# Optimization experiments

Measured on AMD Instinct MI355X. Metric: run time of the kernel, lower is better.

Reference implementation:

```python
import jax, jax.numpy as jnp
import numpy as np

IN_F = 8192
OUT_F = 8192
MAX_STATES = 100
THRESHOLD = MAX_STATES // 2  # 50


def setup_inputs() -> dict:
    key = jax.random.key(0)
    k1, k2 = jax.random.split(key, 2)
    spike_input = (jax.random.uniform(k1, (IN_F,)) < 0.2).astype(jnp.float32)
    # synapse states as in __init__: randn*5 + threshold, clamped to [1, max_states]
    synapse_states = jnp.clip(
        jax.random.normal(k2, (OUT_F, IN_F)) * 5.0 + THRESHOLD, 1.0, float(MAX_STATES)
    ).astype(jnp.float32)
    membrane_potential = jnp.zeros((OUT_F,), jnp.float32)
    adaptive_threshold = jnp.full((OUT_F,), 3.0, jnp.float32)
    eligibility_trace = jnp.zeros((OUT_F, IN_F), jnp.float32)
    refractory_period = jnp.zeros((OUT_F,), jnp.float32)
    return {
        "spike_input": spike_input,
        "synapse_states": synapse_states,
        "membrane_potential": membrane_potential,
        "adaptive_threshold": adaptive_threshold,
        "eligibility_trace": eligibility_trace,
        "refractory_period": refractory_period,
    }


def reference(spike_input, synapse_states, membrane_potential, adaptive_threshold,
              eligibility_trace, refractory_period):
    # Ternary (effectively binary 0/1) weights from synapse states
    w = (synapse_states > float(THRESHOLD)).astype(jnp.float32)  # [out, in]
    x = spike_input.reshape(-1)                                   # [in]
    current = w @ x                                               # [out]
    # LIF membrane update with refractory gating
    v_mem = membrane_potential * 0.5 + current * (1.0 - refractory_period * 0.5)
    spikes = (v_mem >= adaptive_threshold).astype(jnp.float32)    # [out]
    # Eligibility trace: decay + outer-product accumulation + clamp
    new_trace = jnp.clip(eligibility_trace * 0.8 + jnp.outer(spikes, x), 0.0, 5.0)
    # Refractory update
    new_refractory = jnp.clip(refractory_period + spikes - 0.1, 0.0, 1.0)
    # Membrane reset where spiked
    new_membrane = v_mem * (1.0 - spikes)
    return spikes, new_membrane, new_trace, new_refractory
```

## Files before the change

kernel.cpp:

```cpp
#include <hip/hip_runtime.h>


#define IN_F 8192
#define OUT_F 8192
#define BLOCK 256
#define ROW4 (IN_F / 4)
#define CHUNKS (ROW4 / 64)
#define PF 16

typedef float f32x4 __attribute__((ext_vector_type(4)));

__device__ __forceinline__ float dot_step(const f32x4 s, const f32x4 xv) {
    float a = 0.0f;
    a += (s[0] > 50.0f) ? xv[0] : 0.0f;
    a += (s[1] > 50.0f) ? xv[1] : 0.0f;
    a += (s[2] > 50.0f) ? xv[2] : 0.0f;
    a += (s[3] > 50.0f) ? xv[3] : 0.0f;
    return a;
}

__device__ __forceinline__ f32x4 trace_step(const f32x4 t, const f32x4 xv,
                                            const float spike) {
    f32x4 o;
    o[0] = fminf(fmaxf(t[0] * 0.8f + spike * xv[0], 0.0f), 5.0f);
    o[1] = fminf(fmaxf(t[1] * 0.8f + spike * xv[1], 0.0f), 5.0f);
    o[2] = fminf(fmaxf(t[2] * 0.8f + spike * xv[2], 0.0f), 5.0f);
    o[3] = fminf(fmaxf(t[3] * 0.8f + spike * xv[3], 0.0f), 5.0f);
    return o;
}

__global__ __launch_bounds__(BLOCK) void snn_fused_kernel(
    const f32x4* __restrict__ x4,
    const float* __restrict__ syn,
    const float* __restrict__ mem,
    const float* __restrict__ thr,
    const float* __restrict__ refr,
    const f32x4* __restrict__ tr4,
    float* __restrict__ out_spikes,
    float* __restrict__ out_mem,
    float* __restrict__ out_refr,
    f32x4* __restrict__ otr4)
{
    const int wave = threadIdx.x >> 6;
    const int lane = threadIdx.x & 63;
    const int row  = (blockIdx.x << 2) + wave;

    const size_t base4 = (size_t)row * ROW4;
    const f32x4* __restrict__ syn4 = (const f32x4*)syn + base4;
    const f32x4* __restrict__ trR  = tr4  + base4;
    f32x4* __restrict__ otrR       = otr4 + base4;

    const float r_in = refr[row];
    const float m_in = mem[row];
    const float t_in = thr[row];

    f32x4 tbuf[PF];
    #pragma unroll
    for (int it = 0; it < PF; ++it) {
        tbuf[it] = __builtin_nontemporal_load(&trR[(it << 6) + lane]);
    }

    float acc = 0.0f;
    #pragma unroll 8
    for (int it = 0; it < CHUNKS; ++it) {
        const int idx = (it << 6) + lane;
        acc += dot_step(__builtin_nontemporal_load(&syn4[idx]), x4[idx]);
    }

    #pragma unroll
    for (int off = 32; off > 0; off >>= 1)
        acc += __shfl_xor(acc, off, 64);

    const float v     = m_in * 0.5f + acc * (1.0f - r_in * 0.5f);
    const float spike = (v >= t_in) ? 1.0f : 0.0f;
    if (lane == 0) {
        out_spikes[row] = spike;
        out_mem[row]    = v * (1.0f - spike);
        out_refr[row]   = fminf(fmaxf(r_in + spike - 0.1f, 0.0f), 1.0f);
    }

    #pragma unroll
    for (int it = 0; it < PF; ++it) {
        const int idx = (it << 6) + lane;
        __builtin_nontemporal_store(trace_step(tbuf[it], x4[idx], spike),
                                    &otrR[idx]);
    }

    #pragma unroll 8
    for (int it = PF; it < CHUNKS; ++it) {
        const int idx = (it << 6) + lane;
        const f32x4 t = __builtin_nontemporal_load(&trR[idx]);
        __builtin_nontemporal_store(trace_step(t, x4[idx], spike),
                                    &otrR[idx]);
    }
}

extern "C" void kernel_launch(void* const* d_in, const int* in_sizes, int n_in,
                              void* d_out, int out_size, void* d_ws, size_t ws_size,
                              hipStream_t stream) {
    const float* x_in  = (const float*)d_in[0];
    const float* syn   = (const float*)d_in[1];
    const float* mem   = (const float*)d_in[2];
    const float* thr   = (const float*)d_in[3];
    const float* trace = (const float*)d_in[4];
    const float* refr  = (const float*)d_in[5];

    float* out = (float*)d_out;
    float* out_spikes = out;
    float* out_mem    = out + OUT_F;
    float* out_trace  = out + 2 * OUT_F;
    float* out_refr   = out + 2 * OUT_F + (size_t)OUT_F * IN_F;

    snn_fused_kernel<<<OUT_F / 4, BLOCK, 0, stream>>>(
        (const f32x4*)x_in, syn, mem, thr, refr,
        (const f32x4*)trace,
        out_spikes, out_mem, out_refr,
        (f32x4*)out_trace);
}
```

Measured before the change: 575.5 us.

## Pack spike input into per-lane bitmasks and reuse across dot and trace

Each lane reads its slice of the input spike vector once, packs it into four 32-bit bitmasks, and uses those masks both for the binary dot product and for the trace update. This removes the repeated x loads in the trace phase. The trace prefetch depth drops from 16 to 8 vectors to lower register pressure. The change assumes the input is strictly 0/1, which the task specifies, and the kernel stays bound by HBM traffic on the synapse and trace arrays.

```diff
diff --git a/kernel.cpp b/kernel.cpp
--- a/kernel.cpp
+++ b/kernel.cpp
@@ -6,28 +6,56 @@
 #define BLOCK 256
 #define ROW4 (IN_F / 4)
 #define CHUNKS (ROW4 / 64)
-#define PF 16
+#define PF 8
 
 typedef float f32x4 __attribute__((ext_vector_type(4)));
 
-__device__ __forceinline__ float dot_step(const f32x4 s, const f32x4 xv) {
-    float a = 0.0f;
-    a += (s[0] > 50.0f) ? xv[0] : 0.0f;
-    a += (s[1] > 50.0f) ? xv[1] : 0.0f;
-    a += (s[2] > 50.0f) ? xv[2] : 0.0f;
-    a += (s[3] > 50.0f) ? xv[3] : 0.0f;
-    return a;
-}
+#define PACK_BLOCK(O, XM)                                                 \
+    _Pragma("unroll")                                                     \
+    for (int k = 0; k < 8; ++k) {                                         \
+        const f32x4 xv = x4[((((O) << 3) + k) << 6) + lane];              \
+        unsigned b = 0u;                                                  \
+        b |= (xv[0] > 0.5f) ? 1u : 0u;                                    \
+        b |= (xv[1] > 0.5f) ? 2u : 0u;                                    \
+        b |= (xv[2] > 0.5f) ? 4u : 0u;                                    \
+        b |= (xv[3] > 0.5f) ? 8u : 0u;                                    \
+        (XM) |= b << (k * 4);                                             \
+    }
 
-__device__ __forceinline__ f32x4 trace_step(const f32x4 t, const f32x4 xv,
-                                            const float spike) {
-    f32x4 o;
-    o[0] = fminf(fmaxf(t[0] * 0.8f + spike * xv[0], 0.0f), 5.0f);
-    o[1] = fminf(fmaxf(t[1] * 0.8f + spike * xv[1], 0.0f), 5.0f);
-    o[2] = fminf(fmaxf(t[2] * 0.8f + spike * xv[2], 0.0f), 5.0f);
-    o[3] = fminf(fmaxf(t[3] * 0.8f + spike * xv[3], 0.0f), 5.0f);
-    return o;
-}
+#define DOT_BLOCK(O, XM)                                                  \
+    _Pragma("unroll")                                                     \
+    for (int k = 0; k < 8; ++k) {                                         \
+        const int idx = ((((O) << 3) + k) << 6) + lane;                   \
+        const f32x4 s = __builtin_nontemporal_load(&syn4[idx]);           \
+        const unsigned bq = (XM) >> (k * 4);                              \
+        acc += ((s[0] > 50.0f) && (bq & 1u)) ? 1.0f : 0.0f;               \
+        acc += ((s[1] > 50.0f) && (bq & 2u)) ? 1.0f : 0.0f;               \
+        acc += ((s[2] > 50.0f) && (bq & 4u)) ? 1.0f : 0.0f;               \
+        acc += ((s[3] > 50.0f) && (bq & 8u)) ? 1.0f : 0.0f;               \
+    }
+
+#define TRACE_ONE(T, BQ, DST)                                             \
+    {                                                                     \
+        const float s0 = ((BQ) & 1u) ? spike : 0.0f;                      \
+        const float s1 = ((BQ) & 2u) ? spike : 0.0f;                      \
+        const float s2 = ((BQ) & 4u) ? spike : 0.0f;                      \
+        const float s3 = ((BQ) & 8u) ? spike : 0.0f;                      \
+        f32x4 oo;                                                         \
+        oo[0] = fminf(fmaxf((T)[0] * 0.8f + s0, 0.0f), 5.0f);             \
+        oo[1] = fminf(fmaxf((T)[1] * 0.8f + s1, 0.0f), 5.0f);             \
+        oo[2] = fminf(fmaxf((T)[2] * 0.8f + s2, 0.0f), 5.0f);             \
+        oo[3] = fminf(fmaxf((T)[3] * 0.8f + s3, 0.0f), 5.0f);             \
+        __builtin_nontemporal_store(oo, (DST));                           \
+    }
+
+#define TRACE_BLOCK(O, XM)                                                \
+    _Pragma("unroll")                                                     \
+    for (int k = 0; k < 8; ++k) {                                         \
+        const int idx = ((((O) << 3) + k) << 6) + lane;                   \
+        const f32x4 t = __builtin_nontemporal_load(&trR[idx]);            \
+        const unsigned bq = (XM) >> (k * 4);                              \
+        TRACE_ONE(t, bq, &otrR[idx]);                                     \
+    }
 
 __global__ __launch_bounds__(BLOCK) void snn_fused_kernel(
     const f32x4* __restrict__ x4,
@@ -56,16 +84,20 @@
 
     f32x4 tbuf[PF];
     #pragma unroll
-    for (int it = 0; it < PF; ++it) {
-        tbuf[it] = __builtin_nontemporal_load(&trR[(it << 6) + lane]);
-    }
+    for (int k = 0; k < PF; ++k)
+        tbuf[k] = __builtin_nontemporal_load(&trR[(k << 6) + lane]);
+
+    unsigned xm0 = 0u, xm1 = 0u, xm2 = 0u, xm3 = 0u;
+    PACK_BLOCK(0, xm0)
+    PACK_BLOCK(1, xm1)
+    PACK_BLOCK(2, xm2)
+    PACK_BLOCK(3, xm3)
 
     float acc = 0.0f;
-    #pragma unroll 8
-    for (int it = 0; it < CHUNKS; ++it) {
-        const int idx = (it << 6) + lane;
-        acc += dot_step(__builtin_nontemporal_load(&syn4[idx]), x4[idx]);
-    }
+    DOT_BLOCK(0, xm0)
+    DOT_BLOCK(1, xm1)
+    DOT_BLOCK(2, xm2)
+    DOT_BLOCK(3, xm3)
 
     #pragma unroll
     for (int off = 32; off > 0; off >>= 1)
@@ -80,19 +112,15 @@
     }
 
     #pragma unroll
-    for (int it = 0; it < PF; ++it) {
-        const int idx = (it << 6) + lane;
-        __builtin_nontemporal_store(trace_step(tbuf[it], x4[idx], spike),
-                                    &otrR[idx]);
+    for (int k = 0; k < PF; ++k) {
+        const int idx = (k << 6) + lane;
+        const unsigned bq = xm0 >> (k * 4);
+        TRACE_ONE(tbuf[k], bq, &otrR[idx]);
     }
 
-    #pragma unroll 8
-    for (int it = PF; it < CHUNKS; ++it) {
-        const int idx = (it << 6) + lane;
-        const f32x4 t = __builtin_nontemporal_load(&trR[idx]);
-        __builtin_nontemporal_store(trace_step(t, x4[idx], spike),
-                                    &otrR[idx]);
-    }
+    TRACE_BLOCK(1, xm1)
+    TRACE_BLOCK(2, xm2)
+    TRACE_BLOCK(3, xm3)
 }
 
 extern "C" void kernel_launch(void* const* d_in, const int* in_sizes, int n_in,
```

New measurement: 580.5 us. About the same (+0.9%).
